# Performance work log

Hardware: AMD Instinct MI355X
Metric: run time of the kernel (lower is better)

The kernel has to match this reference:

```python
import jax, jax.numpy as jnp
import numpy as np

N_HEAD = 16
TAU = 2.0          # gumbel-softmax temperature
CLAMP = 40.0       # safe_clamp bound for float32
NEG = -1e9         # mask value (stands in for strictly-causal exclusion)


def setup_inputs() -> dict:
    key = jax.random.key(0)
    k1, k2, k3 = jax.random.split(key, 3)
    B, T, E = 2, 2048, 1024
    hidden_states = jax.random.normal(k1, (B, T, E), jnp.float32)
    # nn.MultiheadAttention packed in-projection: rows [0:E]=Q, [E:2E]=K, [2E:3E]=V
    in_proj_weight = jax.random.normal(k2, (3 * E, E), jnp.float32) * 0.02
    in_proj_bias = jax.random.normal(k3, (3 * E,), jnp.float32) * 0.02
    return {
        "hidden_states": hidden_states,
        "in_proj_weight": in_proj_weight,
        "in_proj_bias": in_proj_bias,
    }


def reference(hidden_states, in_proj_weight, in_proj_bias):
    B, T, E = hidden_states.shape
    H = N_HEAD
    D = E // H
    # Only Q/K projections affect the output (attn_out / V / out_proj are discarded
    # by the original module, which uses only the attention weights).
    wq, wk = in_proj_weight[:E], in_proj_weight[E:2 * E]
    bq, bk = in_proj_bias[:E], in_proj_bias[E:2 * E]
    q = (hidden_states @ wq.T + bq).reshape(B, T, H, D)
    k = (hidden_states @ wk.T + bk).reshape(B, T, H, D)

    scale = 1.0 / jnp.sqrt(jnp.float32(D))
    scores = jnp.einsum('bqhd,bkhd->bhqk', q, k) * scale  # [B,H,T,T]

    idx = jnp.arange(T)
    valid = idx[None, :] < idx[:, None]                   # key strictly before query
    scores = jnp.where(valid[None, None], scores, NEG)
    probs = jax.nn.softmax(scores, axis=-1)               # per-head attn weights
    avg = probs.mean(axis=1)                              # average over heads [B,T,T]
    avg = jnp.clip(avg, -CLAMP, CLAMP)                    # safe_clamp (no-op for probs)

    # Gumbel-softmax reweighting (original re-seeds per step from data; here we use
    # a fixed key for deterministic, vectorized sampling).
    logits = jnp.where(valid[None], avg, NEG)
    u = jax.random.uniform(jax.random.key(42), (B, T, T), jnp.float32, 1e-6, 1.0 - 1e-6)
    gumbel = -jnp.log(-jnp.log(u))
    dw = jax.nn.softmax((logits + gumbel) / TAU, axis=-1)  # [B,T,T]

    out = jnp.einsum('btk,bke->bte', dw, hidden_states)    # weighted raw context
    # t == 0 has no context -> zeros
    return jnp.where((idx > 0)[None, :, None], out, 0.0)
```

## Files before the change

### kernel.cpp

```cpp
#include <hip/hip_runtime.h>
#include <math.h>

#define TT 2048
#define EE 1024
#define HH 16
#define DD 64
#define BB 2

typedef __bf16 bf16_t;
typedef __attribute__((ext_vector_type(8))) __bf16 bf16x8;
typedef __attribute__((ext_vector_type(4))) float f32x4;

__device__ __forceinline__ unsigned short f2b(float v) {
    return __builtin_bit_cast(unsigned short, (__bf16)v);
}

__device__ __forceinline__ void gll16(const void* g, void* l) {
    __builtin_amdgcn_global_load_lds(
        (const __attribute__((address_space(1))) void*)g,
        (__attribute__((address_space(3))) void*)l, 16, 0, 0);
}

__device__ __forceinline__ unsigned int rotl32(unsigned int x, int r) {
    return (x << r) | (x >> (32 - r));
}

__device__ __forceinline__ float gumbel_for(unsigned int f) {
    const unsigned int ks0 = 0u;
    const unsigned int ks1 = 42u;
    const unsigned int ks2 = 0x1BD11BDAu ^ ks0 ^ ks1;

    unsigned int v0 = 0u + ks0;
    unsigned int v1 = f  + ks1;

    v0 += v1; v1 = rotl32(v1, 13); v1 ^= v0;
    v0 += v1; v1 = rotl32(v1, 15); v1 ^= v0;
    v0 += v1; v1 = rotl32(v1, 26); v1 ^= v0;
    v0 += v1; v1 = rotl32(v1,  6); v1 ^= v0;
    v0 += ks1; v1 += ks2 + 1u;
    v0 += v1; v1 = rotl32(v1, 17); v1 ^= v0;
    v0 += v1; v1 = rotl32(v1, 29); v1 ^= v0;
    v0 += v1; v1 = rotl32(v1, 16); v1 ^= v0;
    v0 += v1; v1 = rotl32(v1, 24); v1 ^= v0;
    v0 += ks2; v1 += ks0 + 2u;
    v0 += v1; v1 = rotl32(v1, 13); v1 ^= v0;
    v0 += v1; v1 = rotl32(v1, 15); v1 ^= v0;
    v0 += v1; v1 = rotl32(v1, 26); v1 ^= v0;
    v0 += v1; v1 = rotl32(v1,  6); v1 ^= v0;
    v0 += ks0; v1 += ks1 + 3u;
    v0 += v1; v1 = rotl32(v1, 17); v1 ^= v0;
    v0 += v1; v1 = rotl32(v1, 29); v1 ^= v0;
    v0 += v1; v1 = rotl32(v1, 16); v1 ^= v0;
    v0 += v1; v1 = rotl32(v1, 24); v1 ^= v0;
    v0 += ks1; v1 += ks2 + 4u;
    v0 += v1; v1 = rotl32(v1, 13); v1 ^= v0;
    v0 += v1; v1 = rotl32(v1, 15); v1 ^= v0;
    v0 += v1; v1 = rotl32(v1, 26); v1 ^= v0;
    v0 += v1; v1 = rotl32(v1,  6); v1 ^= v0;
    v0 += ks2; v1 += ks0 + 5u;

    unsigned int bits = v0 ^ v1;
    unsigned int fb = (bits >> 9) | 0x3F800000u;
    float u01 = __uint_as_float(fb) - 1.0f;
    const float mn = 1e-6f;
    const float mx = 1.0f - 1e-6f;
    float u = fmaxf(mn, u01 * (mx - mn) + mn);
    return -__logf(-__logf(u));
}

__global__ __launch_bounds__(256) void convert_kernel(
    const float* __restrict__ W, bf16_t* __restrict__ Wbf)
{
    const int total = 2 * EE * EE / 4;
    for (int idx = blockIdx.x * 256 + threadIdx.x; idx < total;
         idx += gridDim.x * 256) {
        float4 v = ((const float4*)W)[idx];
        ushort4 o;
        o.x = f2b(v.x); o.y = f2b(v.y); o.z = f2b(v.z); o.w = f2b(v.w);
        ((ushort4*)Wbf)[idx] = o;
    }
}

__global__ __launch_bounds__(256) void transpose_kernel(
    const float* __restrict__ hs, bf16_t* __restrict__ hsbf,
    bf16_t* __restrict__ hsT)
{
    __shared__ float ts[64][65];
    const int e0 = blockIdx.x * 64;
    const int t0 = blockIdx.y * 64;
    const int b  = blockIdx.z;
    const int tid = threadIdx.x;
#pragma unroll
    for (int it = 0; it < 16; ++it) {
        const int idx = it * 256 + tid;
        const int tr = idx >> 6, te = idx & 63;
        const float v = hs[((size_t)(b * TT + t0 + tr)) * EE + e0 + te];
        ts[tr][te] = v;
        hsbf[((size_t)(b * TT + t0 + tr)) * EE + e0 + te] = (__bf16)v;
    }
    __syncthreads();
#pragma unroll
    for (int it = 0; it < 16; ++it) {
        const int idx = it * 256 + tid;
        const int er = idx >> 6, tc = idx & 63;
        hsT[((size_t)(b * EE + e0 + er)) * TT + t0 + tc] = (__bf16)ts[tc][er];
    }
}

template <int K>
__device__ __forceinline__ void gemm_mainloop(
    const bf16_t* __restrict__ A, const bf16_t* __restrict__ Bm,
    int row0, int col0, int wave, int lane,
    bf16_t* Al0, bf16_t* Al1, bf16_t* Bl0, bf16_t* Bl1,
    f32x4 (&acc)[4][4])
{
    const int lrow = lane & 15;
    const int kgrp = lane >> 4;
    const int wr = wave >> 1, wc = wave & 1;
    const int lr4 = lane >> 2;
    const int sc  = (lane & 3) * 8;

    auto stage = [&](bf16_t* Ald, bf16_t* Bld, int k0) {
#pragma unroll
        for (int c = 0; c < 2; ++c) {
            const int srow = c * 64 + wave * 16;
            gll16(A  + (size_t)(row0 + srow + lr4) * K + k0 + sc, Ald + srow * 32);
            gll16(Bm + (size_t)(col0 + srow + lr4) * K + k0 + sc, Bld + srow * 32);
        }
    };
    auto compute = [&](const bf16_t* Ald, const bf16_t* Bld) {
        bf16x8 af[4], bfr[4];
#pragma unroll
        for (int m = 0; m < 4; ++m)
            af[m] = *(const bf16x8*)(Ald + (wr * 64 + m * 16 + lrow) * 32 + kgrp * 8);
#pragma unroll
        for (int n = 0; n < 4; ++n)
            bfr[n] = *(const bf16x8*)(Bld + (wc * 64 + n * 16 + lrow) * 32 + kgrp * 8);
#pragma unroll
        for (int m = 0; m < 4; ++m)
#pragma unroll
            for (int n = 0; n < 4; ++n)
                acc[m][n] = __builtin_amdgcn_mfma_f32_16x16x32_bf16(
                    af[m], bfr[n], acc[m][n], 0, 0, 0);
    };

    stage(Al0, Bl0, 0);
    __syncthreads();
#pragma unroll 1
    for (int t = 0; t < K / 32; t += 2) {
        stage(Al1, Bl1, (t + 1) * 32);
        compute(Al0, Bl0);
        __syncthreads();
        if (t + 2 < K / 32) stage(Al0, Bl0, (t + 2) * 32);
        compute(Al1, Bl1);
        __syncthreads();
    }
}

__global__ __launch_bounds__(256) void qk_gemm_kernel(
    const bf16_t* __restrict__ hsbf, const bf16_t* __restrict__ Wbf,
    const float* __restrict__ bias,
    bf16_t* __restrict__ Qbf, bf16_t* __restrict__ Kbf)
{
    __shared__ alignas(16) bf16_t Al0[128 * 32], Al1[128 * 32];
    __shared__ alignas(16) bf16_t Bl0[128 * 32], Bl1[128 * 32];

    const int wave = threadIdx.x >> 6;
    const int lane = threadIdx.x & 63;
    const int lrow = lane & 15;
    const int kgrp = lane >> 4;
    const int wr = wave >> 1, wc = wave & 1;
    const int row0 = blockIdx.y * 128;
    const int col0 = blockIdx.x * 128;

    f32x4 acc[4][4] = {};
    gemm_mainloop<EE>(hsbf, Wbf, row0, col0, wave, lane, Al0, Al1, Bl0, Bl1, acc);

#pragma unroll
    for (int n = 0; n < 4; ++n) {
        const int cc = col0 + wc * 64 + n * 16 + lrow;
        const float bv = bias[cc];
#pragma unroll
        for (int m = 0; m < 4; ++m) {
#pragma unroll
            for (int r = 0; r < 4; ++r) {
                const int rr = row0 + wr * 64 + m * 16 + 4 * kgrp + r;
                const float v = acc[m][n][r] + bv;
                const int b = rr >> 11, t = rr & (TT - 1);
                if (cc < EE) {
                    Qbf[(size_t)rr * EE + cc] = (__bf16)v;
                } else {
                    const int h = (cc - EE) >> 6, d = (cc - EE) & 63;
                    Kbf[(((size_t)(b * HH + h)) * TT + t) * DD + d] = (__bf16)v;
                }
            }
        }
    }
}

__global__ __launch_bounds__(256) void out_gemm_kernel(
    const bf16_t* __restrict__ dwbf, const bf16_t* __restrict__ hsT,
    const float* __restrict__ rowinv, float* __restrict__ out)
{
    __shared__ alignas(16) bf16_t Al0[128 * 32], Al1[128 * 32];
    __shared__ alignas(16) bf16_t Bl0[128 * 32], Bl1[128 * 32];

    const int wave = threadIdx.x >> 6;
    const int lane = threadIdx.x & 63;
    const int lrow = lane & 15;
    const int kgrp = lane >> 4;
    const int wr = wave >> 1, wc = wave & 1;
    const int b = blockIdx.z;
    const int row0 = blockIdx.y * 128;
    const int col0 = blockIdx.x * 128;

    const bf16_t* A  = dwbf + (size_t)b * TT * TT;
    const bf16_t* Bm = hsT  + (size_t)b * EE * TT;

    f32x4 acc[4][4] = {};
    gemm_mainloop<TT>(A, Bm, row0, col0, wave, lane, Al0, Al1, Bl0, Bl1, acc);

    float ri[4][4];
#pragma unroll
    for (int m = 0; m < 4; ++m)
#pragma unroll
        for (int r = 0; r < 4; ++r)
            ri[m][r] = rowinv[b * TT + row0 + wr * 64 + m * 16 + 4 * kgrp + r];

#pragma unroll
    for (int n = 0; n < 4; ++n) {
        const int cc = col0 + wc * 64 + n * 16 + lrow;
#pragma unroll
        for (int m = 0; m < 4; ++m) {
#pragma unroll
            for (int r = 0; r < 4; ++r) {
                const int rr = row0 + wr * 64 + m * 16 + 4 * kgrp + r;
                out[(size_t)(b * TT + rr) * EE + cc] = acc[m][n][r] * ri[m][r];
            }
        }
    }
}

__global__ __launch_bounds__(256) void rowsum_kernel(
    const bf16_t* __restrict__ Qbf, const bf16_t* __restrict__ Kbf,
    float* __restrict__ invl_g)
{
    __shared__ float rsp[4][64];
    const int tid = threadIdx.x;
    const int wave = tid >> 6;
    const int lane = tid & 63;
    const int lrow = lane & 15;
    const int kgrp = lane >> 4;
    const int h = blockIdx.y, b = blockIdx.z;
    const bf16_t* Kh = Kbf + (size_t)(b * HH + h) * TT * DD;

#pragma unroll 1
    for (int pick = 0; pick < 2; ++pick) {
        const int it = pick ? (31 - blockIdx.x) : blockIdx.x;
        const int i0 = it * 64;

        bf16x8 af[4][2];
        const bf16_t* qb = Qbf + (size_t)(b * TT + i0 + lrow) * EE + h * DD;
#pragma unroll
        for (int m = 0; m < 4; ++m) {
            af[m][0] = *(const bf16x8*)(qb + (size_t)(m * 16) * EE + kgrp * 8);
            af[m][1] = *(const bf16x8*)(qb + (size_t)(m * 16) * EE + 32 + kgrp * 8);
        }

        f32x4 rs[4] = {};
#pragma unroll 1
        for (int jt = wave; jt <= it; jt += 4) {
            const int j0 = jt * 64;
            const bf16_t* kb = Kh + (size_t)(j0 + lrow) * DD;
            bf16x8 bk[4][2];
#pragma unroll
            for (int n = 0; n < 4; ++n) {
                bk[n][0] = *(const bf16x8*)(kb + (size_t)(n * 16) * DD + kgrp * 8);
                bk[n][1] = *(const bf16x8*)(kb + (size_t)(n * 16) * DD + 32 + kgrp * 8);
            }
#pragma unroll
            for (int m = 0; m < 4; ++m) {
                f32x4 s[4];
#pragma unroll
                for (int n = 0; n < 4; ++n) {
                    s[n] = f32x4{0.f, 0.f, 0.f, 0.f};
                    s[n] = __builtin_amdgcn_mfma_f32_16x16x32_bf16(af[m][0], bk[n][0], s[n], 0, 0, 0);
                    s[n] = __builtin_amdgcn_mfma_f32_16x16x32_bf16(af[m][1], bk[n][1], s[n], 0, 0, 0);
                }
                if (jt == it) {
#pragma unroll
                    for (int n = 0; n < 4; ++n)
#pragma unroll
                        for (int r = 0; r < 4; ++r) {
                            const int jj = j0 + n * 16 + lrow;
                            const int ii = i0 + m * 16 + 4 * kgrp + r;
                            if (jj < ii) rs[m][r] += __expf(0.125f * s[n][r]);
                        }
                } else {
#pragma unroll
                    for (int n = 0; n < 4; ++n)
#pragma unroll
                        for (int r = 0; r < 4; ++r)
                            rs[m][r] += __expf(0.125f * s[n][r]);
                }
            }
        }
#pragma unroll
        for (int off = 1; off < 16; off <<= 1)
#pragma unroll
            for (int m = 0; m < 4; ++m)
#pragma unroll
                for (int r = 0; r < 4; ++r)
                    rs[m][r] += __shfl_xor(rs[m][r], off);
        if (lrow == 0) {
#pragma unroll
            for (int m = 0; m < 4; ++m)
#pragma unroll
                for (int r = 0; r < 4; ++r)
                    rsp[wave][m * 16 + 4 * kgrp + r] = rs[m][r];
        }
        __syncthreads();
        if (tid < 64) {
            const float tot = rsp[0][tid] + rsp[1][tid] + rsp[2][tid] + rsp[3][tid];
            invl_g[(size_t)(b * HH + h) * TT + i0 + tid] =
                (tot > 0.f) ? 1.0f / (tot * (float)HH) : 0.f;
        }
        __syncthreads();
    }
}

__global__ __launch_bounds__(256) void dw_tile_kernel(
    const bf16_t* __restrict__ Qbf, const bf16_t* __restrict__ Kbf,
    const float* __restrict__ invl_g, bf16_t* __restrict__ dwbf)
{
    __shared__ alignas(16) bf16_t kbuf[2][64 * 64];
    __shared__ alignas(16) bf16_t stile[64][72];

    const int wave = threadIdx.x >> 6;
    const int lane = threadIdx.x & 63;
    const int lrow = lane & 15;
    const int kgrp = lane >> 4;
    const int tid = threadIdx.x;
    const int b = blockIdx.y;

    const int tidx = (blockIdx.x & 7) * 66 + (blockIdx.x >> 3);

    int it = (int)((sqrtf(8.0f * tidx + 1.0f) - 1.0f) * 0.5f);
    while ((it + 1) * (it + 2) / 2 <= tidx) ++it;
    while (it * (it + 1) / 2 > tidx) --it;
    const int jt = tidx - it * (it + 1) / 2;
    const bool diag = (it == jt);
    const int i0 = it * 64, j0 = jt * 64;
    const int m = wave;
    const int rbase = i0 + m * 16;
    const int nlim = diag ? (m + 1) : 4;

    int prow[2], pchunk[2];
#pragma unroll
    for (int c = 0; c < 2; ++c) {
        const int p = wave * 2048 + c * 1024 + lane * 16;
        prow[c] = p >> 7;
        pchunk[c] = ((p >> 4) & 7) ^ (prow[c] & 7);
    }
    const bf16_t* Kb0 = Kbf + ((size_t)b * HH * TT + j0) * DD;

    auto stage = [&](int h, int buf) {
#pragma unroll
        for (int c = 0; c < 2; ++c) {
            gll16(Kb0 + (size_t)h * TT * DD + prow[c] * DD + pchunk[c] * 8,
                  (bf16_t*)kbuf[buf] + wave * 1024 + c * 512);
        }
    };

    const bf16_t* qbase = Qbf + (size_t)(b * TT + rbase + lrow) * EE;
    const float*  ribase = invl_g + (size_t)b * HH * TT + rbase + 4 * kgrp;
    const int swz0 = (kgrp ^ (lrow & 7)) * 8;
    const int swz1 = ((4 + kgrp) ^ (lrow & 7)) * 8;

    f32x4 avg[4] = {};

    stage(0, 0);

#pragma unroll 1
    for (int h = 0; h < HH; ++h) {
        const int cur = h & 1;
        const bf16_t* qb = qbase + h * DD;
        const bf16x8 a0 = *(const bf16x8*)(qb + kgrp * 8);
        const bf16x8 a1 = *(const bf16x8*)(qb + 32 + kgrp * 8);
        const f32x4 ric = *(const f32x4*)(ribase + (size_t)h * TT);
        if (h + 1 < HH) stage(h + 1, cur ^ 1);
        asm volatile("s_waitcnt vmcnt(2)" ::: "memory");
        __builtin_amdgcn_s_barrier();

        const bf16_t* kb = kbuf[cur];
        f32x4 s[4];
#pragma unroll
        for (int n = 0; n < 4; ++n) {
            if (n < nlim) {
                const int row = n * 16 + lrow;
                const bf16x8 b0 = *(const bf16x8*)(kb + row * 64 + swz0);
                const bf16x8 b1 = *(const bf16x8*)(kb + row * 64 + swz1);
                s[n] = f32x4{0.f, 0.f, 0.f, 0.f};
                s[n] = __builtin_amdgcn_mfma_f32_16x16x32_bf16(a0, b0, s[n], 0, 0, 0);
                s[n] = __builtin_amdgcn_mfma_f32_16x16x32_bf16(a1, b1, s[n], 0, 0, 0);
            }
        }
#pragma unroll
        for (int n = 0; n < 4; ++n) {
            if (n < nlim) {
#pragma unroll
                for (int r = 0; r < 4; ++r)
                    avg[n][r] += __expf(0.125f * s[n][r]) * ric[r];
            }
        }
        __builtin_amdgcn_s_barrier();
    }

#pragma unroll
    for (int n = 0; n < 4; ++n) {
        const int jj = j0 + n * 16 + lrow;
#pragma unroll
        for (int r = 0; r < 4; ++r) {
            const int rloc = m * 16 + 4 * kgrp + r;
            const int ii = i0 + rloc;
            float val = 0.f;
            if (n < nlim && jj < ii) {
                const float lg = fminf(fmaxf(avg[n][r], -40.0f), 40.0f);
                const float g = gumbel_for((unsigned)(b * TT + ii) * TT + (unsigned)jj);
                val = __expf((lg + g) * 0.5f);
            }
            stile[rloc][n * 16 + lrow] = (__bf16)val;
        }
    }
    __syncthreads();

#pragma unroll
    for (int p = 0; p < 2; ++p) {
        const int idx = p * 256 + tid;
        const int row = idx >> 3, cg = idx & 7;
        *(bf16x8*)(dwbf + (size_t)(b * TT + i0 + row) * TT + j0 + cg * 8) =
            *(const bf16x8*)(&stile[row][cg * 8]);
    }
}

__global__ __launch_bounds__(256) void rowinv_kernel(
    const bf16_t* __restrict__ dwbf, float* __restrict__ rowinv)
{
    __shared__ float red[256];
    const int blk = blockIdx.x;
    const int i = blk & (TT - 1);
    const int tid = threadIdx.x;
    const bf16_t* row = dwbf + (size_t)blk * TT;

    bf16x8 v = *(const bf16x8*)(row + tid * 8);
    float s = 0.f;
#pragma unroll
    for (int e = 0; e < 8; ++e) s += (float)v[e];
    red[tid] = s; __syncthreads();
    for (int st = 128; st > 0; st >>= 1) {
        if (tid < st) red[tid] += red[tid + st];
        __syncthreads();
    }
    if (tid == 0)
        rowinv[blk] = (i > 0 && red[0] > 0.f) ? 1.0f / red[0] : 0.f;
}

extern "C" void kernel_launch(void* const* d_in, const int* in_sizes, int n_in,
                              void* d_out, int out_size, void* d_ws, size_t ws_size,
                              hipStream_t stream) {
    const float* hs   = (const float*)d_in[0];
    const float* W    = (const float*)d_in[1];
    const float* bias = (const float*)d_in[2];
    float* out = (float*)d_out;

    char* ws = (char*)d_ws;
    bf16_t* dwbf   = (bf16_t*)ws;
    bf16_t* Qbf    = (bf16_t*)(ws + (size_t)16 * 1024 * 1024);
    bf16_t* Kbf    = (bf16_t*)(ws + (size_t)24 * 1024 * 1024);
    bf16_t* hsbf   = (bf16_t*)(ws + (size_t)32 * 1024 * 1024);
    bf16_t* Wbf    = (bf16_t*)(ws + (size_t)40 * 1024 * 1024);
    bf16_t* hsT    = (bf16_t*)(ws + (size_t)44 * 1024 * 1024);
    float*  invl_g = (float*) (ws + (size_t)52 * 1024 * 1024);
    float*  rowinv = (float*) (ws + (size_t)52 * 1024 * 1024 + 256 * 1024);

    hipMemsetAsync(dwbf, 0, (size_t)16 * 1024 * 1024, stream);
    convert_kernel<<<1024, 256, 0, stream>>>(W, Wbf);
    transpose_kernel<<<dim3(EE / 64, TT / 64, BB), 256, 0, stream>>>(hs, hsbf, hsT);
    qk_gemm_kernel<<<dim3(2048 / 128, 4096 / 128), 256, 0, stream>>>(hsbf, Wbf, bias, Qbf, Kbf);
    rowsum_kernel<<<dim3(16, HH, BB), 256, 0, stream>>>(Qbf, Kbf, invl_g);
    dw_tile_kernel<<<dim3(528, BB), 256, 0, stream>>>(Qbf, Kbf, invl_g, dwbf);
    rowinv_kernel<<<BB * TT, 256, 0, stream>>>(dwbf, rowinv);
    out_gemm_kernel<<<dim3(EE / 128, TT / 128, BB), 256, 0, stream>>>(dwbf, hsT, rowinv, out);
}
```

Before: 157.1 us.

## Fuse dw row sums via atomics and skip masked K tiles in output GEMM

```diff
diff --git a/kernel.cpp b/kernel.cpp
--- a/kernel.cpp
+++ b/kernel.cpp
@@ -107,10 +107,9 @@
     }
 }
 
-template <int K>
 __device__ __forceinline__ void gemm_mainloop(
     const bf16_t* __restrict__ A, const bf16_t* __restrict__ Bm,
-    int row0, int col0, int wave, int lane,
+    int K, int nt, int row0, int col0, int wave, int lane,
     bf16_t* Al0, bf16_t* Al1, bf16_t* Bl0, bf16_t* Bl1,
     f32x4 (&acc)[4][4])
 {
@@ -147,11 +146,11 @@
     stage(Al0, Bl0, 0);
     __syncthreads();
 #pragma unroll 1
-    for (int t = 0; t < K / 32; t += 2) {
+    for (int t = 0; t < nt; t += 2) {
         stage(Al1, Bl1, (t + 1) * 32);
         compute(Al0, Bl0);
         __syncthreads();
-        if (t + 2 < K / 32) stage(Al0, Bl0, (t + 2) * 32);
+        if (t + 2 < nt) stage(Al0, Bl0, (t + 2) * 32);
         compute(Al1, Bl1);
         __syncthreads();
     }
@@ -174,7 +173,8 @@
     const int col0 = blockIdx.x * 128;
 
     f32x4 acc[4][4] = {};
-    gemm_mainloop<EE>(hsbf, Wbf, row0, col0, wave, lane, Al0, Al1, Bl0, Bl1, acc);
+    gemm_mainloop(hsbf, Wbf, EE, EE / 32, row0, col0, wave, lane,
+                  Al0, Al1, Bl0, Bl1, acc);
 
 #pragma unroll
     for (int n = 0; n < 4; ++n) {
@@ -200,7 +200,7 @@
 
 __global__ __launch_bounds__(256) void out_gemm_kernel(
     const bf16_t* __restrict__ dwbf, const bf16_t* __restrict__ hsT,
-    const float* __restrict__ rowinv, float* __restrict__ out)
+    const float* __restrict__ rsum, float* __restrict__ out)
 {
     __shared__ alignas(16) bf16_t Al0[128 * 32], Al1[128 * 32];
     __shared__ alignas(16) bf16_t Bl0[128 * 32], Bl1[128 * 32];
@@ -218,14 +218,19 @@
     const bf16_t* Bm = hsT  + (size_t)b * EE * TT;
 
     f32x4 acc[4][4] = {};
-    gemm_mainloop<TT>(A, Bm, row0, col0, wave, lane, Al0, Al1, Bl0, Bl1, acc);
+    const int klim = row0 + 128;
+    gemm_mainloop(A, Bm, TT, klim / 32, row0, col0, wave, lane,
+                  Al0, Al1, Bl0, Bl1, acc);
 
     float ri[4][4];
 #pragma unroll
     for (int m = 0; m < 4; ++m)
 #pragma unroll
-        for (int r = 0; r < 4; ++r)
-            ri[m][r] = rowinv[b * TT + row0 + wr * 64 + m * 16 + 4 * kgrp + r];
+        for (int r = 0; r < 4; ++r) {
+            const int rr = row0 + wr * 64 + m * 16 + 4 * kgrp + r;
+            const float s = rsum[b * TT + rr];
+            ri[m][r] = (rr > 0 && s > 0.f) ? 1.0f / s : 0.f;
+        }
 
 #pragma unroll
     for (int n = 0; n < 4; ++n) {
@@ -331,7 +336,8 @@
 
 __global__ __launch_bounds__(256) void dw_tile_kernel(
     const bf16_t* __restrict__ Qbf, const bf16_t* __restrict__ Kbf,
-    const float* __restrict__ invl_g, bf16_t* __restrict__ dwbf)
+    const float* __restrict__ invl_g, bf16_t* __restrict__ dwbf,
+    float* __restrict__ rsum_g)
 {
     __shared__ alignas(16) bf16_t kbuf[2][64 * 64];
     __shared__ alignas(16) bf16_t stile[64][72];
@@ -416,6 +422,7 @@
         __builtin_amdgcn_s_barrier();
     }
 
+    float sr[4] = {0.f, 0.f, 0.f, 0.f};
 #pragma unroll
     for (int n = 0; n < 4; ++n) {
         const int jj = j0 + n * 16 + lrow;
@@ -429,8 +436,18 @@
                 const float g = gumbel_for((unsigned)(b * TT + ii) * TT + (unsigned)jj);
                 val = __expf((lg + g) * 0.5f);
             }
+            sr[r] += val;
             stile[rloc][n * 16 + lrow] = (__bf16)val;
         }
+    }
+#pragma unroll
+    for (int off = 1; off < 16; off <<= 1)
+#pragma unroll
+        for (int r = 0; r < 4; ++r) sr[r] += __shfl_xor(sr[r], off);
+    if (lrow == 0) {
+#pragma unroll
+        for (int r = 0; r < 4; ++r)
+            atomicAdd(&rsum_g[b * TT + rbase + 4 * kgrp + r], sr[r]);
     }
     __syncthreads();
 
@@ -441,28 +458,6 @@
         *(bf16x8*)(dwbf + (size_t)(b * TT + i0 + row) * TT + j0 + cg * 8) =
             *(const bf16x8*)(&stile[row][cg * 8]);
     }
-}
-
-__global__ __launch_bounds__(256) void rowinv_kernel(
-    const bf16_t* __restrict__ dwbf, float* __restrict__ rowinv)
-{
-    __shared__ float red[256];
-    const int blk = blockIdx.x;
-    const int i = blk & (TT - 1);
-    const int tid = threadIdx.x;
-    const bf16_t* row = dwbf + (size_t)blk * TT;
-
-    bf16x8 v = *(const bf16x8*)(row + tid * 8);
-    float s = 0.f;
-#pragma unroll
-    for (int e = 0; e < 8; ++e) s += (float)v[e];
-    red[tid] = s; __syncthreads();
-    for (int st = 128; st > 0; st >>= 1) {
-        if (tid < st) red[tid] += red[tid + st];
-        __syncthreads();
-    }
-    if (tid == 0)
-        rowinv[blk] = (i > 0 && red[0] > 0.f) ? 1.0f / red[0] : 0.f;
 }
 
 extern "C" void kernel_launch(void* const* d_in, const int* in_sizes, int n_in,
@@ -481,14 +476,14 @@
     bf16_t* Wbf    = (bf16_t*)(ws + (size_t)40 * 1024 * 1024);
     bf16_t* hsT    = (bf16_t*)(ws + (size_t)44 * 1024 * 1024);
     float*  invl_g = (float*) (ws + (size_t)52 * 1024 * 1024);
-    float*  rowinv = (float*) (ws + (size_t)52 * 1024 * 1024 + 256 * 1024);
+    float*  rsum_g = (float*) (ws + (size_t)52 * 1024 * 1024 + 256 * 1024);
 
     hipMemsetAsync(dwbf, 0, (size_t)16 * 1024 * 1024, stream);
+    hipMemsetAsync(rsum_g, 0, (size_t)BB * TT * sizeof(float), stream);
     convert_kernel<<<1024, 256, 0, stream>>>(W, Wbf);
     transpose_kernel<<<dim3(EE / 64, TT / 64, BB), 256, 0, stream>>>(hs, hsbf, hsT);
     qk_gemm_kernel<<<dim3(2048 / 128, 4096 / 128), 256, 0, stream>>>(hsbf, Wbf, bias, Qbf, Kbf);
     rowsum_kernel<<<dim3(16, HH, BB), 256, 0, stream>>>(Qbf, Kbf, invl_g);
-    dw_tile_kernel<<<dim3(528, BB), 256, 0, stream>>>(Qbf, Kbf, invl_g, dwbf);
-    rowinv_kernel<<<BB * TT, 256, 0, stream>>>(dwbf, rowinv);
-    out_gemm_kernel<<<dim3(EE / 128, TT / 128, BB), 256, 0, stream>>>(dwbf, hsT, rowinv, out);
-}
+    dw_tile_kernel<<<dim3(528, BB), 256, 0, stream>>>(Qbf, Kbf, invl_g, dwbf, rsum_g);
+    out_gemm_kernel<<<dim3(EE / 128, TT / 128, BB), 256, 0, stream>>>(dwbf, hsT, rsum_g, out);
+}
```

Result: no change. 154.9 us (-1.4%).
